# Performance work log

Hardware: AMD Instinct MI355X
Metric: run time of the kernel (lower is better)

The kernel has to match this reference:

```python
import jax, jax.numpy as jnp
import numpy as np

BIDAT = 4


def _biatt(atoms_vector, amino_vector, U, Wp2c, bp2c, Wc2p, bc2p,
           Whc, bhc, Whp, bhp, Wac, bac, Wap, bap, Wcc, bcc, Wcp, bcp):
    cfs, pfs = [], []
    for i in range(BIDAT):  # fixed small structural loop (4 distinct param sets)
        # bilinear tanh affinity: [Na, Np]
        A = jnp.tanh((atoms_vector @ U[i]) @ amino_vector.T)
        atoms_trans = A @ jnp.tanh(amino_vector @ Wp2c[i] + bp2c[i])      # [Na, D]
        amino_trans = A.T @ jnp.tanh(atoms_vector @ Wc2p[i] + bc2p[i])    # [Np, D]
        atoms_tmp = jnp.concatenate(
            [jnp.tanh(atoms_vector @ Whc[i] + bhc[i]), atoms_trans], axis=1)  # [Na, 2D]
        amino_tmp = jnp.concatenate(
            [jnp.tanh(amino_vector @ Whp[i] + bhp[i]), amino_trans], axis=1)  # [Np, 2D]
        # NOTE: softmax over axis=1 of a [N,1] tensor == all-ones (faithful to torch source)
        atoms_att = jax.nn.softmax(atoms_tmp @ Wac[i] + bac[i], axis=1)   # [Na, 1]
        amino_att = jax.nn.softmax(amino_tmp @ Wap[i] + bap[i], axis=1)   # [Np, 1]
        cfs.append(atoms_vector * atoms_att)
        pfs.append(amino_vector * amino_att)
    cf_final = jnp.concatenate(cfs, axis=1) @ Wcc + bcc   # [Na, D]
    pf_final = jnp.concatenate(pfs, axis=1) @ Wcp + bcp   # [Np, D]
    return cf_final, pf_final


def setup_inputs() -> dict:
    D, Na, Np = 512, 6144, 6144
    key = jax.random.key(0)
    ks = jax.random.split(key, 20)
    s = 0.04  # ~xavier-scale init for D=512
    return {
        "atoms_vector": jax.random.normal(ks[0], (Na, D), jnp.float32),
        "amino_vector": jax.random.normal(ks[1], (Np, D), jnp.float32),
        "U":    jax.random.normal(ks[2], (BIDAT, D, D), jnp.float32) * s,
        "Wp2c": jax.random.normal(ks[3], (BIDAT, D, D), jnp.float32) * s,
        "bp2c": jnp.zeros((BIDAT, D), jnp.float32),
        "Wc2p": jax.random.normal(ks[4], (BIDAT, D, D), jnp.float32) * s,
        "bc2p": jnp.zeros((BIDAT, D), jnp.float32),
        "Whc":  jax.random.normal(ks[5], (BIDAT, D, D), jnp.float32) * s,
        "bhc":  jnp.zeros((BIDAT, D), jnp.float32),
        "Whp":  jax.random.normal(ks[6], (BIDAT, D, D), jnp.float32) * s,
        "bhp":  jnp.zeros((BIDAT, D), jnp.float32),
        "Wac":  jax.random.normal(ks[7], (BIDAT, 2 * D, 1), jnp.float32) * s,
        "bac":  jnp.zeros((BIDAT, 1), jnp.float32),
        "Wap":  jax.random.normal(ks[8], (BIDAT, 2 * D, 1), jnp.float32) * s,
        "bap":  jnp.zeros((BIDAT, 1), jnp.float32),
        "Wcc":  jax.random.normal(ks[9], (BIDAT * D, D), jnp.float32) * s,
        "bcc":  jnp.zeros((D,), jnp.float32),
        "Wcp":  jax.random.normal(ks[10], (BIDAT * D, D), jnp.float32) * s,
        "bcp":  jnp.zeros((D,), jnp.float32),
    }


def reference(atoms_vector, amino_vector, U, Wp2c, bp2c, Wc2p, bc2p,
              Whc, bhc, Whp, bhp, Wac, bac, Wap, bap, Wcc, bcc, Wcp, bcp):
    return _biatt(atoms_vector, amino_vector, U, Wp2c, bp2c, Wc2p, bc2p,
                  Whc, bhc, Whp, bhp, Wac, bac, Wap, bap, Wcc, bcc, Wcp, bcp)
```

## Files before the change

### kernel.cpp

```cpp
#include <hip/hip_runtime.h>
#include <hip/hip_bf16.h>

#define DDIM 512
#define NROWS 6144
#define BM 64
#define BN 64
#define BK 32
#define KSTEPS (DDIM / BK)

typedef __attribute__((ext_vector_type(8))) short short8;
typedef __attribute__((ext_vector_type(4))) float f32x4;

#define GLDS16(g, s)                                          \
  __builtin_amdgcn_global_load_lds(                           \
      (const __attribute__((address_space(1))) void*)(g),     \
      (__attribute__((address_space(3))) void*)(s), 16, 0, 0)

__global__ __launch_bounds__(256) void prep_w(
    const float* __restrict__ Wcc, const float* __restrict__ Wcp,
    __hip_bfloat16* __restrict__ Wt) {
    const float* W = blockIdx.z ? Wcp : Wcc;
    unsigned short* o = (unsigned short*)Wt + (size_t)blockIdx.z * DDIM * DDIM;
    __shared__ float lds[32][65];
    const int k0 = blockIdx.x * 32, n0 = blockIdx.y * 64;
    #pragma unroll
    for (int u = 0; u < 2; ++u) {
        int idx = u * 256 + threadIdx.x;
        int kk = idx >> 4, c = idx & 15;
        float4 s = {0.f, 0.f, 0.f, 0.f};
        #pragma unroll
        for (int i = 0; i < 4; ++i) {
            float4 v = *(const float4*)&W[(size_t)(i * DDIM + k0 + kk) * DDIM + n0 + c * 4];
            s.x += v.x; s.y += v.y; s.z += v.z; s.w += v.w;
        }
        lds[kk][c * 4 + 0] = s.x;
        lds[kk][c * 4 + 1] = s.y;
        lds[kk][c * 4 + 2] = s.z;
        lds[kk][c * 4 + 3] = s.w;
    }
    __syncthreads();
    #pragma unroll
    for (int u = 0; u < 2; ++u) {
        int idx = u * 256 + threadIdx.x;
        int nr = idx >> 3, kc = idx & 7;
        ushort4 p;
        #pragma unroll
        for (int j = 0; j < 4; ++j) {
            __hip_bfloat16 h = __float2bfloat16(lds[kc * 4 + j][nr]);
            ((unsigned short*)&p)[j] = *(unsigned short*)&h;
        }
        *(ushort4*)&o[(size_t)(n0 + nr) * DDIM + k0 + kc * 4] = p;
    }
}

__global__ __launch_bounds__(256, 2) void gemm_bias(
    const float* __restrict__ Aat, const float* __restrict__ Aam,
    const __hip_bfloat16* __restrict__ Wtall,
    const float* __restrict__ bias0, const float* __restrict__ bias1,
    float* __restrict__ C) {
  __shared__ unsigned short Bs[BN * DDIM];
  __shared__ float As[2][BM * BK];

  const int z = blockIdx.z;
  const float* A = z ? Aam : Aat;
  const unsigned short* Wt = (const unsigned short*)Wtall + (size_t)z * DDIM * DDIM;
  const float* bias = z ? bias1 : bias0;
  float* Cz = C + (size_t)z * NROWS * DDIM;

  const int tid = threadIdx.x;
  const int w = tid >> 6, l = tid & 63;
  const int lr = l & 15, hi = l >> 4;
  const int m0 = blockIdx.x * BM, n0 = blockIdx.y * BN;

  #pragma unroll
  for (int r = 0; r < 16; ++r) {
    const int row = w * 16 + r;
    GLDS16(Wt + (size_t)(n0 + row) * DDIM + ((l ^ (row & 7)) << 3),
           &Bs[row * DDIM]);
  }

  const int ra0 = w * 16 + (l >> 3), ra1 = ra0 + 8;
  const float* srcA0 = A + (size_t)(m0 + ra0) * DDIM + (((l & 7) ^ (ra0 & 7)) << 2);
  const float* srcA1 = A + (size_t)(m0 + ra1) * DDIM + (((l & 7) ^ (ra1 & 7)) << 2);
  const unsigned ldsA0 = (w * 16) * BK, ldsA1 = (w * 16 + 8) * BK;

#define STAGE(buf, kk)                              \
  do {                                              \
    GLDS16(srcA0 + (kk) * BK, &As[buf][ldsA0]);     \
    GLDS16(srcA1 + (kk) * BK, &As[buf][ldsA1]);     \
  } while (0)

  STAGE(0, 0);
  STAGE(1, 1);

  f32x4 acc[4];
  #pragma unroll
  for (int j = 0; j < 4; ++j) acc[j] = (f32x4){0.f, 0.f, 0.f, 0.f};

  asm volatile("s_waitcnt vmcnt(4)" ::: "memory");
  __builtin_amdgcn_s_barrier();

  #pragma unroll
  for (int t = 0; t < KSTEPS; ++t) {
    if (t < KSTEPS - 1)
      asm volatile("s_waitcnt vmcnt(2)" ::: "memory");
    else
      asm volatile("s_waitcnt vmcnt(0)" ::: "memory");
    const int buf = t & 1;

    const int r = w * 16 + lr;
    f32x4 x0 = *(const f32x4*)&As[buf][r * BK + (((hi * 2 + 0) ^ (lr & 7)) << 2)];
    f32x4 x1 = *(const f32x4*)&As[buf][r * BK + (((hi * 2 + 1) ^ (lr & 7)) << 2)];
    short8 af;
    {
      float xv[8] = {x0[0], x0[1], x0[2], x0[3], x1[0], x1[1], x1[2], x1[3]};
      #pragma unroll
      for (int e = 0; e < 8; ++e) {
        __hip_bfloat16 h = __float2bfloat16(xv[e]);
        af[e] = *(short*)&h;
      }
    }
    #pragma unroll
    for (int tn = 0; tn < 4; ++tn) {
      const int np = tn * 16 + lr;
      const int slot = (t * 4 + hi) ^ (lr & 7);
      short8 bf = *(const short8*)&Bs[np * DDIM + slot * 8];
      acc[tn] = __builtin_amdgcn_mfma_f32_16x16x32_bf16(af, bf, acc[tn], 0, 0, 0);
    }

    if (t + 2 < KSTEPS) {
      asm volatile("s_waitcnt lgkmcnt(0)" ::: "memory");
      __builtin_amdgcn_sched_barrier(0);
      STAGE(buf, t + 2);
    }
  }

  #pragma unroll
  for (int tn = 0; tn < 4; ++tn) {
    const int col = n0 + tn * 16 + lr;
    const float bv = bias[col];
    #pragma unroll
    for (int rr = 0; rr < 4; ++rr)
      Cz[(size_t)(m0 + w * 16 + hi * 4 + rr) * DDIM + col] = acc[tn][rr] + bv;
  }
#undef STAGE
}

extern "C" void kernel_launch(void* const* d_in, const int* in_sizes, int n_in,
                              void* d_out, int out_size, void* d_ws, size_t ws_size,
                              hipStream_t stream) {
    const float* atoms = (const float*)d_in[0];
    const float* amino = (const float*)d_in[1];
    const float* Wcc   = (const float*)d_in[15];
    const float* bcc   = (const float*)d_in[16];
    const float* Wcp   = (const float*)d_in[17];
    const float* bcp   = (const float*)d_in[18];
    float* out = (float*)d_out;

    __hip_bfloat16* Wt = (__hip_bfloat16*)d_ws;

    dim3 fgrid(DDIM / 32, DDIM / 64, 2);
    prep_w<<<fgrid, 256, 0, stream>>>(Wcc, Wcp, Wt);

    dim3 ggrid(NROWS / BM, DDIM / BN, 2);
    gemm_bias<<<ggrid, 256, 0, stream>>>(atoms, amino, Wt, bcc, bcp, out);
}
```

Before: 147.2 us.

## Stream B tiles per k-step with triple-buffered bf16 LDS and 2x2 wave tiling

Stops preloading the whole 64x512 bf16 weight panel into LDS. Each k-step now streams small A and B tiles through triple-buffered LDS. A is loaded into registers, converted to bf16 once and written to shared memory. Each wave computes a 32x32 sub-tile from fragments shared across waves, so each thread converts less A. LDS use drops so the launch bound allows more resident blocks, at the cost of a barrier every k-step.

```diff
diff --git a/kernel.cpp b/kernel.cpp
--- a/kernel.cpp
+++ b/kernel.cpp
@@ -6,7 +6,7 @@
 #define BM 64
 #define BN 64
 #define BK 32
-#define KSTEPS (DDIM / BK)
+#define KSTEPS 16
 
 typedef __attribute__((ext_vector_type(8))) short short8;
 typedef __attribute__((ext_vector_type(4))) float f32x4;
@@ -53,13 +53,13 @@
     }
 }
 
-__global__ __launch_bounds__(256, 2) void gemm_bias(
+__global__ __launch_bounds__(256, 6) void gemm_bias(
     const float* __restrict__ Aat, const float* __restrict__ Aam,
     const __hip_bfloat16* __restrict__ Wtall,
     const float* __restrict__ bias0, const float* __restrict__ bias1,
     float* __restrict__ C) {
-  __shared__ unsigned short Bs[BN * DDIM];
-  __shared__ float As[2][BM * BK];
+  __shared__ unsigned short As[3][BM * BK];
+  __shared__ unsigned short Bs[3][BN * BK];
 
   const int z = blockIdx.z;
   const float* A = z ? Aam : Aat;
@@ -70,80 +70,88 @@
   const int tid = threadIdx.x;
   const int w = tid >> 6, l = tid & 63;
   const int lr = l & 15, hi = l >> 4;
+  const int wm = w >> 1, wn = w & 1;
   const int m0 = blockIdx.x * BM, n0 = blockIdx.y * BN;
 
+  const int sr = w * 16 + (l >> 2);
+  const int sc = l & 3;
+  const float* srcA = A + (size_t)(m0 + sr) * DDIM + sc * 8;
+  const unsigned short* srcB =
+      Wt + (size_t)(n0 + sr) * DDIM + ((sc ^ ((sr >> 1) & 3)) << 3);
+  const unsigned ldsB = (unsigned)(w * 16 * BK);
+  const unsigned wrA = (unsigned)(sr * BK + ((sc ^ ((sr >> 1) & 3)) << 3));
+
+  const int ar0 = wm * 32 + lr, ar1 = ar0 + 16;
+  const int br0 = wn * 32 + lr, br1 = br0 + 16;
+  const unsigned adA0 = ar0 * BK + ((hi ^ ((ar0 >> 1) & 3)) << 3);
+  const unsigned adA1 = ar1 * BK + ((hi ^ ((ar1 >> 1) & 3)) << 3);
+  const unsigned adB0 = br0 * BK + ((hi ^ ((br0 >> 1) & 3)) << 3);
+  const unsigned adB1 = br1 * BK + ((hi ^ ((br1 >> 1) & 3)) << 3);
+
+  f32x4 acc[2][2];
   #pragma unroll
-  for (int r = 0; r < 16; ++r) {
-    const int row = w * 16 + r;
-    GLDS16(Wt + (size_t)(n0 + row) * DDIM + ((l ^ (row & 7)) << 3),
-           &Bs[row * DDIM]);
-  }
+  for (int i = 0; i < 2; ++i)
+    #pragma unroll
+    for (int j = 0; j < 2; ++j) acc[i][j] = (f32x4){0.f, 0.f, 0.f, 0.f};
 
-  const int ra0 = w * 16 + (l >> 3), ra1 = ra0 + 8;
-  const float* srcA0 = A + (size_t)(m0 + ra0) * DDIM + (((l & 7) ^ (ra0 & 7)) << 2);
-  const float* srcA1 = A + (size_t)(m0 + ra1) * DDIM + (((l & 7) ^ (ra1 & 7)) << 2);
-  const unsigned ldsA0 = (w * 16) * BK, ldsA1 = (w * 16 + 8) * BK;
+  float4 rA[2][2];
 
-#define STAGE(buf, kk)                              \
-  do {                                              \
-    GLDS16(srcA0 + (kk) * BK, &As[buf][ldsA0]);     \
-    GLDS16(srcA1 + (kk) * BK, &As[buf][ldsA1]);     \
-  } while (0)
-
-  STAGE(0, 0);
-  STAGE(1, 1);
-
-  f32x4 acc[4];
-  #pragma unroll
-  for (int j = 0; j < 4; ++j) acc[j] = (f32x4){0.f, 0.f, 0.f, 0.f};
-
-  asm volatile("s_waitcnt vmcnt(4)" ::: "memory");
-  __builtin_amdgcn_s_barrier();
+  rA[0][0] = *(const float4*)(srcA + 0 * BK);
+  rA[0][1] = *(const float4*)(srcA + 0 * BK + 4);
+  GLDS16(srcB + 0 * BK, &Bs[0][ldsB]);
+  rA[1][0] = *(const float4*)(srcA + 1 * BK);
+  rA[1][1] = *(const float4*)(srcA + 1 * BK + 4);
+  GLDS16(srcB + 1 * BK, &Bs[1][ldsB]);
 
   #pragma unroll
   for (int t = 0; t < KSTEPS; ++t) {
     if (t < KSTEPS - 1)
-      asm volatile("s_waitcnt vmcnt(2)" ::: "memory");
+      asm volatile("s_waitcnt vmcnt(3)" ::: "memory");
     else
       asm volatile("s_waitcnt vmcnt(0)" ::: "memory");
-    const int buf = t & 1;
 
-    const int r = w * 16 + lr;
-    f32x4 x0 = *(const f32x4*)&As[buf][r * BK + (((hi * 2 + 0) ^ (lr & 7)) << 2)];
-    f32x4 x1 = *(const f32x4*)&As[buf][r * BK + (((hi * 2 + 1) ^ (lr & 7)) << 2)];
-    short8 af;
     {
-      float xv[8] = {x0[0], x0[1], x0[2], x0[3], x1[0], x1[1], x1[2], x1[3]};
+      const float4 x0 = rA[t & 1][0], x1 = rA[t & 1][1];
+      const float xv[8] = {x0.x, x0.y, x0.z, x0.w, x1.x, x1.y, x1.z, x1.w};
+      short8 av;
       #pragma unroll
       for (int e = 0; e < 8; ++e) {
         __hip_bfloat16 h = __float2bfloat16(xv[e]);
-        af[e] = *(short*)&h;
+        av[e] = *(short*)&h;
       }
+      *(short8*)&As[t % 3][wrA] = av;
     }
-    #pragma unroll
-    for (int tn = 0; tn < 4; ++tn) {
-      const int np = tn * 16 + lr;
-      const int slot = (t * 4 + hi) ^ (lr & 7);
-      short8 bf = *(const short8*)&Bs[np * DDIM + slot * 8];
-      acc[tn] = __builtin_amdgcn_mfma_f32_16x16x32_bf16(af, bf, acc[tn], 0, 0, 0);
+    if (t + 2 < KSTEPS) {
+      rA[t & 1][0] = *(const float4*)(srcA + (t + 2) * BK);
+      rA[t & 1][1] = *(const float4*)(srcA + (t + 2) * BK + 4);
     }
+    asm volatile("s_waitcnt lgkmcnt(0)" ::: "memory");
+    __builtin_amdgcn_s_barrier();
+    if (t + 2 < KSTEPS)
+      GLDS16(srcB + (t + 2) * BK, &Bs[(t + 2) % 3][ldsB]);
 
-    if (t + 2 < KSTEPS) {
-      asm volatile("s_waitcnt lgkmcnt(0)" ::: "memory");
-      __builtin_amdgcn_sched_barrier(0);
-      STAGE(buf, t + 2);
-    }
+    short8 af0 = *(const short8*)&As[t % 3][adA0];
+    short8 af1 = *(const short8*)&As[t % 3][adA1];
+    short8 bf0 = *(const short8*)&Bs[t % 3][adB0];
+    short8 bf1 = *(const short8*)&Bs[t % 3][adB1];
+    acc[0][0] = __builtin_amdgcn_mfma_f32_16x16x32_bf16(af0, bf0, acc[0][0], 0, 0, 0);
+    acc[0][1] = __builtin_amdgcn_mfma_f32_16x16x32_bf16(af0, bf1, acc[0][1], 0, 0, 0);
+    acc[1][0] = __builtin_amdgcn_mfma_f32_16x16x32_bf16(af1, bf0, acc[1][0], 0, 0, 0);
+    acc[1][1] = __builtin_amdgcn_mfma_f32_16x16x32_bf16(af1, bf1, acc[1][1], 0, 0, 0);
   }
 
   #pragma unroll
-  for (int tn = 0; tn < 4; ++tn) {
-    const int col = n0 + tn * 16 + lr;
+  for (int tn = 0; tn < 2; ++tn) {
+    const int col = n0 + wn * 32 + tn * 16 + lr;
     const float bv = bias[col];
     #pragma unroll
-    for (int rr = 0; rr < 4; ++rr)
-      Cz[(size_t)(m0 + w * 16 + hi * 4 + rr) * DDIM + col] = acc[tn][rr] + bv;
+    for (int tm = 0; tm < 2; ++tm) {
+      const int row = m0 + wm * 32 + tm * 16 + hi * 4;
+      #pragma unroll
+      for (int r = 0; r < 4; ++r)
+        Cz[(size_t)(row + r) * DDIM + col] = acc[tm][tn][r] + bv;
+    }
   }
-#undef STAGE
 }
 
 extern "C" void kernel_launch(void* const* d_in, const int* in_sizes, int n_in,
```

New measurement: 144.0 us. -2.2%, faster.
